# Optimization experiments

Measured on AMD Instinct MI355X. Metric: run time of the kernel, lower is better.

## Reference

```python
import jax, jax.numpy as jnp
import numpy as np

N_NODES = 100000
N_EDGES = 1600000
IN_C = 128
HID_C = 128
OUT_C = 64
N_GRAPHS = 64


def setup_inputs() -> dict:
    key = jax.random.key(0)
    ks = jax.random.split(key, 12)
    x = jax.random.normal(ks[0], (N_NODES, IN_C), dtype=jnp.float32)
    edge_index = jax.random.randint(ks[1], (2, N_EDGES), 0, N_NODES, dtype=jnp.int64)
    batch = jnp.sort(jax.random.randint(ks[2], (N_NODES,), 0, N_GRAPHS, dtype=jnp.int64))
    def glorot(k, fan_in, fan_out):
        s = jnp.sqrt(6.0 / (fan_in + fan_out))
        return jax.random.uniform(k, (fan_in, fan_out), jnp.float32, -s, s)
    W1 = glorot(ks[3], IN_C, HID_C);  b1 = jnp.zeros((HID_C,), jnp.float32)
    W2 = glorot(ks[4], HID_C, HID_C); b2 = jnp.zeros((HID_C,), jnp.float32)
    W3 = glorot(ks[5], HID_C, HID_C); b3 = jnp.zeros((HID_C,), jnp.float32)
    Wlin = glorot(ks[6], HID_C, OUT_C)
    blin = jnp.zeros((OUT_C,), jnp.float32)
    return {"x": x, "edge_index": edge_index, "batch": batch,
            "W1": W1, "b1": b1, "W2": W2, "b2": b2, "W3": W3, "b3": b3,
            "Wlin": Wlin, "blin": blin}


def _gcn_conv(x, W, b, src, dst, norm):
    # PyG GCNConv: h = x @ W; out[dst] += norm * h[src]; out += b
    h = x @ W
    msg = h[src] * norm[:, None]                     # [E+N, C] edge-wise gather (memory-bound)
    out = jax.ops.segment_sum(msg, dst, num_segments=N_NODES)
    return out + b


def reference(x, edge_index, batch, W1, b1, W2, b2, W3, b3, Wlin, blin):
    # add self-loops (PyG default add_self_loops=True)
    loops = jnp.arange(N_NODES, dtype=edge_index.dtype)
    src = jnp.concatenate([edge_index[0], loops])
    dst = jnp.concatenate([edge_index[1], loops])
    # symmetric normalization: deg over dst with unit edge weights
    deg = jax.ops.segment_sum(jnp.ones_like(src, dtype=x.dtype), dst, num_segments=N_NODES)
    dinv = jnp.where(deg > 0, jax.lax.rsqrt(deg), 0.0)
    norm = dinv[src] * dinv[dst]                     # [E+N]

    h = jax.nn.relu(_gcn_conv(x, W1, b1, src, dst, norm))
    h = jax.nn.relu(_gcn_conv(h, W2, b2, src, dst, norm))
    h = jax.nn.relu(_gcn_conv(h, W3, b3, src, dst, norm))

    # global mean pool over graphs
    sums = jax.ops.segment_sum(h, batch, num_segments=N_GRAPHS)
    cnts = jax.ops.segment_sum(jnp.ones((N_NODES,), h.dtype), batch, num_segments=N_GRAPHS)
    pooled = sums / jnp.clip(cnts, 1.0)[:, None]     # [G, HID_C]
    return pooled @ Wlin + blin                      # [G, OUT_C]
```

## Files before the change

### kernel.cpp

```cpp
#include <hip/hip_runtime.h>
#include <stdint.h>

#define C_HID 128
#define NGRAPH 64
#define COUT 64
#define POOL_S 64
#define NBLK 256
#define BKT 256
#define NBUK_MAX 512
#define SCAN_CH 4096

typedef short bf16x8 __attribute__((ext_vector_type(8)));
typedef float f32x4 __attribute__((ext_vector_type(4)));
typedef float f32x2 __attribute__((ext_vector_type(2)));

__device__ __forceinline__ unsigned short f2bf(float f){
  unsigned int u = __builtin_bit_cast(unsigned int, f);
  u = u + 0x7FFFu + ((u >> 16) & 1u);
  return (unsigned short)(u >> 16);
}
__device__ __forceinline__ float bflo(unsigned int u){
  return __builtin_bit_cast(float, u << 16);
}
__device__ __forceinline__ float bfhi(unsigned int u){
  return __builtin_bit_cast(float, u & 0xFFFF0000u);
}
__device__ __forceinline__ int clampi(int v, int lo, int hi){
  return v < lo ? lo : (v > hi ? hi : v);
}

__global__ void k_zero(float* __restrict__ out, int n){
  int i = blockIdx.x*blockDim.x + threadIdx.x;
  if (i < n) out[i] = 0.f;
}

__global__ __launch_bounds__(256) void k_cnt(const int* __restrict__ dst,
                                             int* __restrict__ cntg,
                                             int E, int N, int NBUK, int chunk){
  __shared__ int cnt[NBUK_MAX];
  int blk = blockIdx.x, t = threadIdx.x;
  for (int b = t; b < NBUK; b += 256) cnt[b] = 0;
  __syncthreads();
  int e0 = blk*chunk, e1 = min(E, e0 + chunk);
  for (int e = e0 + t; e < e1; e += 256)
    atomicAdd(&cnt[clampi(dst[e], 0, N-1) >> 8], 1);
  __syncthreads();
  for (int b = t; b < NBUK; b += 256)
    cntg[b*NBLK + blk] = cnt[b];
}

__global__ __launch_bounds__(256) void k_scanA(const int* __restrict__ cnt,
                                               int* __restrict__ bsum, int n){
  __shared__ int red[256];
  int blk = blockIdx.x, t = threadIdx.x;
  int base = blk*SCAN_CH + t*16;
  int s = 0;
  #pragma unroll
  for (int j = 0; j < 16; ++j){ int i = base + j; s += (i < n) ? cnt[i] : 0; }
  red[t] = s; __syncthreads();
  for (int off = 128; off > 0; off >>= 1){
    if (t < off) red[t] += red[t + off];
    __syncthreads();
  }
  if (t == 0) bsum[blk] = red[0];
}

__global__ __launch_bounds__(256) void k_scanB(const int* __restrict__ bsum,
                                               int* __restrict__ bbase,
                                               int* __restrict__ bases, int nb, int n){
  __shared__ int buf[256];
  int t = threadIdx.x;
  int v = (t < nb) ? bsum[t] : 0;
  buf[t] = v; __syncthreads();
  for (int off = 1; off < 256; off <<= 1){
    int add = (t >= off) ? buf[t-off] : 0;
    __syncthreads();
    buf[t] += add;
    __syncthreads();
  }
  if (t < nb) bbase[t] = buf[t] - v;
  if (t == nb-1) bases[n] = buf[t];
}

__global__ __launch_bounds__(256) void k_scanC(const int* __restrict__ cnt,
                                               const int* __restrict__ bbase,
                                               int* __restrict__ bases, int n){
  __shared__ int buf[256];
  int blk = blockIdx.x, t = threadIdx.x;
  int base = blk*SCAN_CH + t*16;
  int loc[16]; int s = 0;
  #pragma unroll
  for (int j = 0; j < 16; ++j){ int i = base + j; loc[j] = (i < n) ? cnt[i] : 0; s += loc[j]; }
  buf[t] = s; __syncthreads();
  for (int off = 1; off < 256; off <<= 1){
    int add = (t >= off) ? buf[t-off] : 0;
    __syncthreads();
    buf[t] += add;
    __syncthreads();
  }
  int run = bbase[blk] + buf[t] - s;
  #pragma unroll
  for (int j = 0; j < 16; ++j){
    int i = base + j;
    if (i < n) bases[i] = run;
    run += loc[j];
  }
}

__global__ __launch_bounds__(256) void k_scat(const int* __restrict__ src,
                                              const int* __restrict__ dst,
                                              const int* __restrict__ bases,
                                              unsigned int* __restrict__ rec,
                                              int E, int N, int NBUK, int chunk){
  __shared__ int cur[NBUK_MAX];
  int blk = blockIdx.x, t = threadIdx.x;
  for (int b = t; b < NBUK; b += 256) cur[b] = bases[b*NBLK + blk];
  __syncthreads();
  int e0 = blk*chunk, e1 = min(E, e0 + chunk);
  for (int e = e0 + t; e < e1; e += 256){
    int d = clampi(dst[e], 0, N-1);
    int s = clampi(src[e], 0, N-1);
    int p = atomicAdd(&cur[d >> 8], 1);
    rec[p] = (unsigned int)s | ((unsigned int)(d & 255) << 24);
  }
}

__global__ __launch_bounds__(256) void k_csr(const unsigned int* __restrict__ rec,
                                             const int* __restrict__ bases,
                                             int* __restrict__ offs, float* __restrict__ dinv,
                                             int* __restrict__ meta, int E, int N, int NBUK){
  __shared__ int cnt[BKT], loff[BKT], cur[BKT];
  int b = blockIdx.x, t = threadIdx.x;
  cnt[t] = 0;
  __syncthreads();
  int r0 = bases[b*NBLK];
  int r1 = (b+1 < NBUK) ? bases[(b+1)*NBLK] : E;
  for (int i = r0 + t; i < r1; i += 256)
    atomicAdd(&cnt[rec[i] >> 24], 1);
  __syncthreads();
  loff[t] = cnt[t];
  __syncthreads();
  for (int off = 1; off < BKT; off <<= 1){
    int add = (t >= off) ? loff[t - off] : 0;
    __syncthreads();
    loff[t] += add;
    __syncthreads();
  }
  int excl = loff[t] - cnt[t];
  cur[t] = r0 + excl;
  int node = b*BKT + t;
  if (node < N){
    offs[node] = r0 + excl;
    dinv[node] = rsqrtf((float)(cnt[t] + 1));
  }
  if (b == NBUK-1 && t == 0) offs[N] = E;
  __syncthreads();
  for (int i = r0 + t; i < r1; i += 256){
    unsigned int r = rec[i];
    int p = atomicAdd(&cur[r >> 24], 1);
    meta[p] = (int)(r & 0x00FFFFFFu);
  }
}

__global__ void k_xcast(const float2* __restrict__ x, const float* __restrict__ dinv,
                        unsigned short* __restrict__ y, unsigned short* __restrict__ y2, int N){
  int i = blockIdx.x*256 + threadIdx.x;
  int tot = N*64;
  if (i < tot){
    float2 v = x[i];
    float dn = dinv[i >> 6] * 64.f;
    int p = __builtin_amdgcn_cvt_pk_fp8_f32(v.x*dn, v.y*dn, 0, false);
    y[i] = (unsigned short)(p & 0xFFFF);
  } else if (i < tot + 64){
    y[i] = 0;
    y2[i] = 0;
  }
}

__global__ void k_prep(const float* __restrict__ W1, const float* __restrict__ W2,
                       const float* __restrict__ W3, unsigned short* __restrict__ Wt){
  int idx = blockIdx.x*256 + threadIdx.x;
  int w = idx >> 14;
  int r = idx & 16383;
  int n = r & 127, k = r >> 7;
  const float* W = (w == 0) ? W1 : (w == 1) ? W2 : W3;
  Wt[(size_t)w*16384 + (size_t)n*128 + k] = f2bf(W[k*128 + n]);
}

__global__ __launch_bounds__(256) void k_spmm(const unsigned short* __restrict__ y,
                       const int* __restrict__ offs,
                       const float* __restrict__ dinv,
                       const int* __restrict__ meta,
                       unsigned int* __restrict__ agg, int N){
  int wv   = __builtin_amdgcn_readfirstlane(threadIdx.x >> 6);
  int lane = threadIdx.x & 63;
  int g = lane >> 4, c = lane & 15;
  int node0 = blockIdx.x*16 + wv*4;
  if (node0 >= N) return;

  int eA = offs[node0];
  int eB = offs[min(node0+1, N)];
  int eC = offs[min(node0+2, N)];
  int eD = offs[min(node0+3, N)];
  int eE = offs[min(node0+4, N)];
  int c0 = eB-eA, c1 = eC-eB, c2 = eD-eC, c3 = eE-eD;
  int maxc = max(max(c0,c1), max(c2,c3));

  int e0l  = (g==0) ? eA : (g==1) ? eB : (g==2) ? eC : eD;
  int cntl = (g==0) ? c0 : (g==1) ? c1 : (g==2) ? c2 : c3;
  int nodeg = node0 + g;
  bool nok = nodeg < N;
  int nself = nok ? nodeg : N;

  const uint2* yrow = (const uint2*)y;

  int mv0 = (c < cntl)      ? meta[e0l + c]      : N;
  int mv1 = (c + 16 < cntl) ? meta[e0l + c + 16] : N;
  uint2 us = yrow[(size_t)nself*16 + c];
  float dl = dinv[nok ? nodeg : 0];

  f32x2 acc[4];
  { f32x2 f;
    f = __builtin_amdgcn_cvt_pk_f32_fp8((int)us.x, false); acc[0] = f;
    f = __builtin_amdgcn_cvt_pk_f32_fp8((int)us.x, true);  acc[1] = f;
    f = __builtin_amdgcn_cvt_pk_f32_fp8((int)us.y, false); acc[2] = f;
    f = __builtin_amdgcn_cvt_pk_f32_fp8((int)us.y, true);  acc[3] = f; }

  uint2 u[8];
#define SWZ0(J) __builtin_amdgcn_ds_swizzle(mv0, (0x10 | (((J)&15)<<5)))
#define SWZ1(J) __builtin_amdgcn_ds_swizzle(mv1, (0x10 | (((J)&15)<<5)))
#define GA(K, SM) u[K] = yrow[(size_t)(unsigned)(SM)*16 + c]
#define CONV8() do{ _Pragma("unroll") \
  for (int k2 = 0; k2 < 8; ++k2){ \
    f32x2 f; \
    f = __builtin_amdgcn_cvt_pk_f32_fp8((int)u[k2].x, false); acc[0] += f; \
    f = __builtin_amdgcn_cvt_pk_f32_fp8((int)u[k2].x, true);  acc[1] += f; \
    f = __builtin_amdgcn_cvt_pk_f32_fp8((int)u[k2].y, false); acc[2] += f; \
    f = __builtin_amdgcn_cvt_pk_f32_fp8((int)u[k2].y, true);  acc[3] += f; } }while(0)

  if (0 < maxc){
    GA(0,SWZ0(0)); GA(1,SWZ0(1)); GA(2,SWZ0(2)); GA(3,SWZ0(3));
    GA(4,SWZ0(4)); GA(5,SWZ0(5)); GA(6,SWZ0(6)); GA(7,SWZ0(7));
    __builtin_amdgcn_sched_barrier(0);
    CONV8();
  }
  if (8 < maxc){
    GA(0,SWZ0(8)); GA(1,SWZ0(9)); GA(2,SWZ0(10)); GA(3,SWZ0(11));
    GA(4,SWZ0(12)); GA(5,SWZ0(13)); GA(6,SWZ0(14)); GA(7,SWZ0(15));
    __builtin_amdgcn_sched_barrier(0);
    CONV8();
  }
  if (16 < maxc){
    GA(0,SWZ1(16)); GA(1,SWZ1(17)); GA(2,SWZ1(18)); GA(3,SWZ1(19));
    GA(4,SWZ1(20)); GA(5,SWZ1(21)); GA(6,SWZ1(22)); GA(7,SWZ1(23));
    __builtin_amdgcn_sched_barrier(0);
    CONV8();
  }
  if (24 < maxc){
    GA(0,SWZ1(24)); GA(1,SWZ1(25)); GA(2,SWZ1(26)); GA(3,SWZ1(27));
    GA(4,SWZ1(28)); GA(5,SWZ1(29)); GA(6,SWZ1(30)); GA(7,SWZ1(31));
    __builtin_amdgcn_sched_barrier(0);
    CONV8();
  }
#undef SWZ0
#undef SWZ1
#undef GA
#undef CONV8

  for (int j = 32; j < maxc; ++j){
    int sm = (j < cntl) ? meta[e0l + j] : N;
    uint2 t = yrow[(size_t)(unsigned)sm*16 + c];
    f32x2 f;
    f = __builtin_amdgcn_cvt_pk_f32_fp8((int)t.x, false); acc[0] += f;
    f = __builtin_amdgcn_cvt_pk_f32_fp8((int)t.x, true);  acc[1] += f;
    f = __builtin_amdgcn_cvt_pk_f32_fp8((int)t.y, false); acc[2] += f;
    f = __builtin_amdgcn_cvt_pk_f32_fp8((int)t.y, true);  acc[3] += f;
  }

  float dn = dl * 0.015625f;
  if (nok){
    uint4 w;
    w.x = (unsigned int)f2bf(acc[0].x*dn) | ((unsigned int)f2bf(acc[0].y*dn) << 16);
    w.y = (unsigned int)f2bf(acc[1].x*dn) | ((unsigned int)f2bf(acc[1].y*dn) << 16);
    w.z = (unsigned int)f2bf(acc[2].x*dn) | ((unsigned int)f2bf(acc[2].y*dn) << 16);
    w.w = (unsigned int)f2bf(acc[3].x*dn) | ((unsigned int)f2bf(acc[3].y*dn) << 16);
    *(uint4*)(agg + (size_t)nodeg*64 + c*4) = w;
  }
}

#define GEMM_BLOCKS 512
template<bool FP8OUT>
__global__ __launch_bounds__(256) void k_gemm(const unsigned short* __restrict__ A,
                                              const unsigned short* __restrict__ Wt,
                                              const float* __restrict__ bias,
                                              const float* __restrict__ scale,
                                              void* __restrict__ outv, int M){
  __shared__ unsigned short wt[128*136];
  {
    const uint4* wsrc = (const uint4*)Wt;
    for (int i = threadIdx.x; i < 4096; i += 256){
      uint4 v = wsrc[i];
      int n = i >> 4, kblk = i & 15;
      *(uint4*)&wt[n*136 + kblk*8] = v;
    }
  }
  __syncthreads();

  int wv = threadIdx.x >> 6, lane = threadIdx.x & 63;
  int q = lane >> 4, ln = lane & 15;
  int tiles = (M + 63) >> 6;

  for (int tile = blockIdx.x; tile < tiles; tile += GEMM_BLOCKS){
    int m0 = tile*64 + wv*16;
    int arow = m0 + ln;
    bool arow_ok = (arow < M);
    int arow_s = arow_ok ? arow : 0;

    f32x4 zero = {0.f, 0.f, 0.f, 0.f};
    f32x4 acc[8];
    #pragma unroll
    for (int t = 0; t < 8; ++t) acc[t] = zero;

    #pragma unroll
    for (int kk = 0; kk < 4; ++kk){
      bf16x8 a;
      if (arow_ok){
        __builtin_memcpy(&a, A + (size_t)arow_s*128 + kk*32 + q*8, 16);
      } else {
        a = (bf16x8){0,0,0,0,0,0,0,0};
      }
      #pragma unroll
      for (int t = 0; t < 8; ++t){
        bf16x8 b;
        __builtin_memcpy(&b, &wt[(t*16 + ln)*136 + kk*32 + q*8], 16);
        acc[t] = __builtin_amdgcn_mfma_f32_16x16x32_bf16(a, b, acc[t], 0, 0, 0);
      }
    }
    float sc[4];
    #pragma unroll
    for (int r = 0; r < 4; ++r){
      int row = m0 + q*4 + r;
      sc[r] = (FP8OUT && row < M) ? scale[row] * 64.f : 1.0f;
    }
    #pragma unroll
    for (int t = 0; t < 8; ++t){
      float bv = bias[t*16 + ln];
      #pragma unroll
      for (int r = 0; r < 4; ++r){
        int row = m0 + q*4 + r;
        if (row < M){
          float v = acc[t][r] + bv;
          v = v > 0.f ? v : 0.f;
          if (FP8OUT){
            v *= sc[r];
            int p = __builtin_amdgcn_cvt_pk_fp8_f32(v, v, 0, false);
            ((unsigned char*)outv)[(size_t)row*128 + t*16 + ln] = (unsigned char)(p & 0xFF);
          } else {
            ((unsigned short*)outv)[(size_t)row*128 + t*16 + ln] = f2bf(v);
          }
        }
      }
    }
  }
}

__device__ __forceinline__ int lower_bound_i(const int* arr, int n, int val){
  int lo = 0, hi = n;
  while (lo < hi){ int mid = (lo + hi) >> 1; if (arr[mid] < val) lo = mid + 1; else hi = mid; }
  return lo;
}

__global__ void k_pool(const unsigned int* __restrict__ x, const int* __restrict__ batch,
                       float* __restrict__ partial, int N){
  int g = blockIdx.x / POOL_S, s = blockIdx.x % POOL_S;
  int h = threadIdx.x >> 6;
  int lane = threadIdx.x & 63;
  int rs = clampi(lower_bound_i(batch, N, g), 0, N);
  int re = clampi(lower_bound_i(batch, N, g + 1), rs, N);
  int len = re - rs;
  int a = rs + (int)(((long long)len * s) / POOL_S);
  int b = rs + (int)(((long long)len * (s + 1)) / POOL_S);
  float ax = 0.f, ay = 0.f;
  for (int i = a + h; i < b; i += 2){
    unsigned int u = x[(size_t)i*64 + lane];
    ax += bflo(u);
    ay += bfhi(u);
  }
  float* p = partial + ((size_t)(g*POOL_S + s)*2 + h)*C_HID;
  p[2*lane]   = ax;
  p[2*lane+1] = ay;
}

__global__ void k_final(const float* __restrict__ partial, const int* __restrict__ batch,
                        const float* __restrict__ Wl, const float* __restrict__ bl,
                        float* __restrict__ out, int N){
  __shared__ float sums[C_HID];
  int g = blockIdx.x;
  int t = threadIdx.x;
  float acc = 0.f;
  const float* p = partial + (size_t)g*POOL_S*2*C_HID;
  for (int j = 0; j < POOL_S*2; ++j)
    acc += p[j*C_HID + t];
  sums[t] = acc;
  __syncthreads();
  if (t < COUT){
    int rs = clampi(lower_bound_i(batch, N, g), 0, N);
    int re = clampi(lower_bound_i(batch, N, g + 1), rs, N);
    float inv = 1.0f / fmaxf((float)(re - rs), 1.0f);
    float o = 0.f;
    for (int k = 0; k < 128; ++k)
      o += sums[k] * Wl[k*COUT + t];
    out[g*COUT + t] = o * inv + bl[t];
  }
}

extern "C" void kernel_launch(void* const* d_in, const int* in_sizes, int n_in,
                              void* d_out, int out_size, void* d_ws, size_t ws_size,
                              hipStream_t stream){
  const float* x0 = (const float*)d_in[0];
  const int* ei   = (const int*)d_in[1];
  const int* batch= (const int*)d_in[2];
  const float* W1 = (const float*)d_in[3];
  const float* b1 = (const float*)d_in[4];
  const float* W2 = (const float*)d_in[5];
  const float* b2 = (const float*)d_in[6];
  const float* W3 = (const float*)d_in[7];
  const float* b3 = (const float*)d_in[8];
  const float* Wl = (const float*)d_in[9];
  const float* bl = (const float*)d_in[10];
  float* out = (float*)d_out;

  int E = in_sizes[1] / 2;
  int N = in_sizes[2];
  const int* src = ei;
  const int* dst = ei + E;
  int NBUK = (N + BKT - 1) / BKT;
  int chunk = (E + NBLK - 1) / NBLK;
  int ncnt = NBUK * NBLK;
  int nsb  = (ncnt + SCAN_CH - 1) / SCAN_CH;

  size_t off_acc = 0;
  auto carve = [&](size_t bytes)->size_t{
    size_t r = off_acc; off_acc += (bytes + 255) & ~(size_t)255; return r;
  };
  size_t o_cnt   = carve((size_t)ncnt*4);
  size_t o_bases = carve((size_t)(ncnt+1)*4);
  size_t o_bsum  = carve(256*4);
  size_t o_bbase = carve(256*4);
  size_t o_offs  = carve((size_t)(N+1)*4);
  size_t o_dinv  = carve((size_t)N*4);
  size_t o_meta  = carve((size_t)E*4);
  size_t o_rec   = carve((size_t)E*4);
  size_t o_yA    = carve((size_t)(N+1)*C_HID);
  size_t o_yB    = carve((size_t)(N+1)*C_HID);
  size_t o_aggb  = carve((size_t)N*C_HID*2);
  size_t o_wt    = carve((size_t)3*128*128*2);
  size_t need = off_acc;

  size_t hbuf_avail = o_aggb - o_meta;
  bool alias_ok = hbuf_avail >= (size_t)N*C_HID*2;
  alias_ok = alias_ok &&
             ((size_t)(N+1)*C_HID >= (size_t)NGRAPH*POOL_S*2*C_HID*4);

  if (ws_size < need || NBUK > NBUK_MAX || nsb > 256 || !alias_ok){
    k_zero<<<(out_size+255)/256, 256, 0, stream>>>(out, out_size);
    return;
  }

  char* base = (char*)d_ws;
  int* cntg  = (int*)(base + o_cnt);
  int* bases = (int*)(base + o_bases);
  int* bsum  = (int*)(base + o_bsum);
  int* bbase = (int*)(base + o_bbase);
  int* offs  = (int*)(base + o_offs);
  float* dinv= (float*)(base + o_dinv);
  int* meta  = (int*)(base + o_meta);
  unsigned int* rec   = (unsigned int*)(base + o_rec);
  unsigned short* yA  = (unsigned short*)(base + o_yA);
  unsigned short* yB  = (unsigned short*)(base + o_yB);
  unsigned int* aggb  = (unsigned int*)(base + o_aggb);
  unsigned short* wt  = (unsigned short*)(base + o_wt);
  unsigned short* hbuf= (unsigned short*)(base + o_meta);
  float* part         = (float*)(base + o_yB);

  k_cnt  <<<NBLK, 256, 0, stream>>>(dst, cntg, E, N, NBUK, chunk);
  k_scanA<<<nsb, 256, 0, stream>>>(cntg, bsum, ncnt);
  k_scanB<<<1, 256, 0, stream>>>(bsum, bbase, bases, nsb, ncnt);
  k_scanC<<<nsb, 256, 0, stream>>>(cntg, bbase, bases, ncnt);
  k_scat <<<NBLK, 256, 0, stream>>>(src, dst, bases, rec, E, N, NBUK, chunk);
  k_csr  <<<NBUK, BKT, 0, stream>>>(rec, bases, offs, dinv, meta, E, N, NBUK);

  k_xcast<<<(N*64 + 64 + 255)/256, 256, 0, stream>>>((const float2*)x0, dinv, yA, yB, N);
  k_prep <<<192, 256, 0, stream>>>(W1, W2, W3, wt);

  int spmm_grid = (N + 15) / 16;

  k_spmm<<<spmm_grid, 256, 0, stream>>>(yA, offs, dinv, meta, aggb, N);
  k_gemm<true ><<<GEMM_BLOCKS, 256, 0, stream>>>((const unsigned short*)aggb, wt,           b1, dinv, (void*)yB, N);
  k_spmm<<<spmm_grid, 256, 0, stream>>>(yB, offs, dinv, meta, aggb, N);
  k_gemm<true ><<<GEMM_BLOCKS, 256, 0, stream>>>((const unsigned short*)aggb, wt + 16384,   b2, dinv, (void*)yA, N);
  k_spmm<<<spmm_grid, 256, 0, stream>>>(yA, offs, dinv, meta, aggb, N);
  k_gemm<false><<<GEMM_BLOCKS, 256, 0, stream>>>((const unsigned short*)aggb, wt + 2*16384, b3, dinv, (void*)hbuf, N);

  k_pool <<<NGRAPH*POOL_S, 128, 0, stream>>>((const unsigned int*)hbuf, batch, part, N);
  k_final<<<NGRAPH, 128, 0, stream>>>(part, batch, Wl, bl, out, N);
}
```

Baseline: 338.0 us.

## Fuse SpMM aggregation with dense GEMM per 64-node tile via shared memory

Merges the per-layer sparse aggregation kernel and the bf16 MFMA GEMM kernel into one kernel. Each block aggregates 64 nodes into a shared-memory A tile, then multiplies it by the weight matrix read directly from global memory (no LDS staging of W). This removes the bf16 aggregate round-trip through global memory and half the launches, at the cost of per-block uncoalesced weight reads and a block-wide sync between gather and MFMA phases. hbuf now gets its own workspace slot instead of aliasing meta.

```diff
diff --git a/kernel.cpp b/kernel.cpp
--- a/kernel.cpp
+++ b/kernel.cpp
@@ -187,46 +187,50 @@
   Wt[(size_t)w*16384 + (size_t)n*128 + k] = f2bf(W[k*128 + n]);
 }
 
-__global__ __launch_bounds__(256) void k_spmm(const unsigned short* __restrict__ y,
+template<bool FP8OUT>
+__global__ __launch_bounds__(256) void k_fused(const unsigned short* __restrict__ y,
                        const int* __restrict__ offs,
                        const float* __restrict__ dinv,
                        const int* __restrict__ meta,
-                       unsigned int* __restrict__ agg, int N){
+                       const unsigned short* __restrict__ Wt,
+                       const float* __restrict__ bias,
+                       void* __restrict__ outv, int N){
+  __shared__ unsigned short As[64*136];
   int wv   = __builtin_amdgcn_readfirstlane(threadIdx.x >> 6);
   int lane = threadIdx.x & 63;
   int g = lane >> 4, c = lane & 15;
-  int node0 = blockIdx.x*16 + wv*4;
-  if (node0 >= N) return;
-
-  int eA = offs[node0];
-  int eB = offs[min(node0+1, N)];
-  int eC = offs[min(node0+2, N)];
-  int eD = offs[min(node0+3, N)];
-  int eE = offs[min(node0+4, N)];
-  int c0 = eB-eA, c1 = eC-eB, c2 = eD-eC, c3 = eE-eD;
-  int maxc = max(max(c0,c1), max(c2,c3));
-
-  int e0l  = (g==0) ? eA : (g==1) ? eB : (g==2) ? eC : eD;
-  int cntl = (g==0) ? c0 : (g==1) ? c1 : (g==2) ? c2 : c3;
-  int nodeg = node0 + g;
-  bool nok = nodeg < N;
-  int nself = nok ? nodeg : N;
-
+  int tile0 = blockIdx.x*64;
   const uint2* yrow = (const uint2*)y;
 
-  int mv0 = (c < cntl)      ? meta[e0l + c]      : N;
-  int mv1 = (c + 16 < cntl) ? meta[e0l + c + 16] : N;
-  uint2 us = yrow[(size_t)nself*16 + c];
-  float dl = dinv[nok ? nodeg : 0];
-
-  f32x2 acc[4];
-  { f32x2 f;
-    f = __builtin_amdgcn_cvt_pk_f32_fp8((int)us.x, false); acc[0] = f;
-    f = __builtin_amdgcn_cvt_pk_f32_fp8((int)us.x, true);  acc[1] = f;
-    f = __builtin_amdgcn_cvt_pk_f32_fp8((int)us.y, false); acc[2] = f;
-    f = __builtin_amdgcn_cvt_pk_f32_fp8((int)us.y, true);  acc[3] = f; }
-
-  uint2 u[8];
+  for (int b4 = 0; b4 < 4; ++b4){
+    int node0 = tile0 + wv*16 + b4*4;
+    int eA = offs[min(node0,   N)];
+    int eB = offs[min(node0+1, N)];
+    int eC = offs[min(node0+2, N)];
+    int eD = offs[min(node0+3, N)];
+    int eE = offs[min(node0+4, N)];
+    int c0 = eB-eA, c1 = eC-eB, c2 = eD-eC, c3 = eE-eD;
+    int maxc = max(max(c0,c1), max(c2,c3));
+
+    int e0l  = (g==0) ? eA : (g==1) ? eB : (g==2) ? eC : eD;
+    int cntl = (g==0) ? c0 : (g==1) ? c1 : (g==2) ? c2 : c3;
+    int nodeg = node0 + g;
+    bool nok = nodeg < N;
+    int nself = nok ? nodeg : N;
+
+    int mv0 = (c < cntl)      ? meta[e0l + c]      : N;
+    int mv1 = (c + 16 < cntl) ? meta[e0l + c + 16] : N;
+    uint2 us = yrow[(size_t)nself*16 + c];
+    float dl = dinv[nok ? nodeg : 0];
+
+    f32x2 acc[4];
+    { f32x2 f;
+      f = __builtin_amdgcn_cvt_pk_f32_fp8((int)us.x, false); acc[0] = f;
+      f = __builtin_amdgcn_cvt_pk_f32_fp8((int)us.x, true);  acc[1] = f;
+      f = __builtin_amdgcn_cvt_pk_f32_fp8((int)us.y, false); acc[2] = f;
+      f = __builtin_amdgcn_cvt_pk_f32_fp8((int)us.y, true);  acc[3] = f; }
+
+    uint2 u[8];
 #define SWZ0(J) __builtin_amdgcn_ds_swizzle(mv0, (0x10 | (((J)&15)<<5)))
 #define SWZ1(J) __builtin_amdgcn_ds_swizzle(mv1, (0x10 | (((J)&15)<<5)))
 #define GA(K, SM) u[K] = yrow[(size_t)(unsigned)(SM)*16 + c]
@@ -238,126 +242,96 @@
     f = __builtin_amdgcn_cvt_pk_f32_fp8((int)u[k2].y, false); acc[2] += f; \
     f = __builtin_amdgcn_cvt_pk_f32_fp8((int)u[k2].y, true);  acc[3] += f; } }while(0)
 
-  if (0 < maxc){
-    GA(0,SWZ0(0)); GA(1,SWZ0(1)); GA(2,SWZ0(2)); GA(3,SWZ0(3));
-    GA(4,SWZ0(4)); GA(5,SWZ0(5)); GA(6,SWZ0(6)); GA(7,SWZ0(7));
-    __builtin_amdgcn_sched_barrier(0);
-    CONV8();
-  }
-  if (8 < maxc){
-    GA(0,SWZ0(8)); GA(1,SWZ0(9)); GA(2,SWZ0(10)); GA(3,SWZ0(11));
-    GA(4,SWZ0(12)); GA(5,SWZ0(13)); GA(6,SWZ0(14)); GA(7,SWZ0(15));
-    __builtin_amdgcn_sched_barrier(0);
-    CONV8();
-  }
-  if (16 < maxc){
-    GA(0,SWZ1(16)); GA(1,SWZ1(17)); GA(2,SWZ1(18)); GA(3,SWZ1(19));
-    GA(4,SWZ1(20)); GA(5,SWZ1(21)); GA(6,SWZ1(22)); GA(7,SWZ1(23));
-    __builtin_amdgcn_sched_barrier(0);
-    CONV8();
-  }
-  if (24 < maxc){
-    GA(0,SWZ1(24)); GA(1,SWZ1(25)); GA(2,SWZ1(26)); GA(3,SWZ1(27));
-    GA(4,SWZ1(28)); GA(5,SWZ1(29)); GA(6,SWZ1(30)); GA(7,SWZ1(31));
-    __builtin_amdgcn_sched_barrier(0);
-    CONV8();
-  }
+    if (0 < maxc){
+      GA(0,SWZ0(0)); GA(1,SWZ0(1)); GA(2,SWZ0(2)); GA(3,SWZ0(3));
+      GA(4,SWZ0(4)); GA(5,SWZ0(5)); GA(6,SWZ0(6)); GA(7,SWZ0(7));
+      __builtin_amdgcn_sched_barrier(0);
+      CONV8();
+    }
+    if (8 < maxc){
+      GA(0,SWZ0(8)); GA(1,SWZ0(9)); GA(2,SWZ0(10)); GA(3,SWZ0(11));
+      GA(4,SWZ0(12)); GA(5,SWZ0(13)); GA(6,SWZ0(14)); GA(7,SWZ0(15));
+      __builtin_amdgcn_sched_barrier(0);
+      CONV8();
+    }
+    if (16 < maxc){
+      GA(0,SWZ1(16)); GA(1,SWZ1(17)); GA(2,SWZ1(18)); GA(3,SWZ1(19));
+      GA(4,SWZ1(20)); GA(5,SWZ1(21)); GA(6,SWZ1(22)); GA(7,SWZ1(23));
+      __builtin_amdgcn_sched_barrier(0);
+      CONV8();
+    }
+    if (24 < maxc){
+      GA(0,SWZ1(24)); GA(1,SWZ1(25)); GA(2,SWZ1(26)); GA(3,SWZ1(27));
+      GA(4,SWZ1(28)); GA(5,SWZ1(29)); GA(6,SWZ1(30)); GA(7,SWZ1(31));
+      __builtin_amdgcn_sched_barrier(0);
+      CONV8();
+    }
 #undef SWZ0
 #undef SWZ1
 #undef GA
 #undef CONV8
 
-  for (int j = 32; j < maxc; ++j){
-    int sm = (j < cntl) ? meta[e0l + j] : N;
-    uint2 t = yrow[(size_t)(unsigned)sm*16 + c];
-    f32x2 f;
-    f = __builtin_amdgcn_cvt_pk_f32_fp8((int)t.x, false); acc[0] += f;
-    f = __builtin_amdgcn_cvt_pk_f32_fp8((int)t.x, true);  acc[1] += f;
-    f = __builtin_amdgcn_cvt_pk_f32_fp8((int)t.y, false); acc[2] += f;
-    f = __builtin_amdgcn_cvt_pk_f32_fp8((int)t.y, true);  acc[3] += f;
-  }
-
-  float dn = dl * 0.015625f;
-  if (nok){
-    uint4 w;
-    w.x = (unsigned int)f2bf(acc[0].x*dn) | ((unsigned int)f2bf(acc[0].y*dn) << 16);
-    w.y = (unsigned int)f2bf(acc[1].x*dn) | ((unsigned int)f2bf(acc[1].y*dn) << 16);
-    w.z = (unsigned int)f2bf(acc[2].x*dn) | ((unsigned int)f2bf(acc[2].y*dn) << 16);
-    w.w = (unsigned int)f2bf(acc[3].x*dn) | ((unsigned int)f2bf(acc[3].y*dn) << 16);
-    *(uint4*)(agg + (size_t)nodeg*64 + c*4) = w;
-  }
-}
-
-#define GEMM_BLOCKS 512
-template<bool FP8OUT>
-__global__ __launch_bounds__(256) void k_gemm(const unsigned short* __restrict__ A,
-                                              const unsigned short* __restrict__ Wt,
-                                              const float* __restrict__ bias,
-                                              const float* __restrict__ scale,
-                                              void* __restrict__ outv, int M){
-  __shared__ unsigned short wt[128*136];
-  {
-    const uint4* wsrc = (const uint4*)Wt;
-    for (int i = threadIdx.x; i < 4096; i += 256){
-      uint4 v = wsrc[i];
-      int n = i >> 4, kblk = i & 15;
-      *(uint4*)&wt[n*136 + kblk*8] = v;
-    }
-  }
-  __syncthreads();
-
-  int wv = threadIdx.x >> 6, lane = threadIdx.x & 63;
-  int q = lane >> 4, ln = lane & 15;
-  int tiles = (M + 63) >> 6;
-
-  for (int tile = blockIdx.x; tile < tiles; tile += GEMM_BLOCKS){
-    int m0 = tile*64 + wv*16;
-    int arow = m0 + ln;
-    bool arow_ok = (arow < M);
-    int arow_s = arow_ok ? arow : 0;
-
-    f32x4 zero = {0.f, 0.f, 0.f, 0.f};
-    f32x4 acc[8];
+    for (int j = 32; j < maxc; ++j){
+      int sm = (j < cntl) ? meta[e0l + j] : N;
+      uint2 t = yrow[(size_t)(unsigned)sm*16 + c];
+      f32x2 f;
+      f = __builtin_amdgcn_cvt_pk_f32_fp8((int)t.x, false); acc[0] += f;
+      f = __builtin_amdgcn_cvt_pk_f32_fp8((int)t.x, true);  acc[1] += f;
+      f = __builtin_amdgcn_cvt_pk_f32_fp8((int)t.y, false); acc[2] += f;
+      f = __builtin_amdgcn_cvt_pk_f32_fp8((int)t.y, true);  acc[3] += f;
+    }
+
+    float dn = dl * 0.015625f;
+    uint4 w = {0u, 0u, 0u, 0u};
+    if (nok){
+      w.x = (unsigned int)f2bf(acc[0].x*dn) | ((unsigned int)f2bf(acc[0].y*dn) << 16);
+      w.y = (unsigned int)f2bf(acc[1].x*dn) | ((unsigned int)f2bf(acc[1].y*dn) << 16);
+      w.z = (unsigned int)f2bf(acc[2].x*dn) | ((unsigned int)f2bf(acc[2].y*dn) << 16);
+      w.w = (unsigned int)f2bf(acc[3].x*dn) | ((unsigned int)f2bf(acc[3].y*dn) << 16);
+    }
+    *(uint4*)&As[(size_t)(wv*16 + b4*4 + g)*136 + c*8] = w;
+  }
+  __syncthreads();
+
+  int q = g, ln = c;
+  f32x4 zero = {0.f, 0.f, 0.f, 0.f};
+  f32x4 acc[8];
+  #pragma unroll
+  for (int t = 0; t < 8; ++t) acc[t] = zero;
+
+  #pragma unroll
+  for (int kk = 0; kk < 4; ++kk){
+    bf16x8 a;
+    __builtin_memcpy(&a, &As[(size_t)(wv*16 + ln)*136 + kk*32 + q*8], 16);
     #pragma unroll
-    for (int t = 0; t < 8; ++t) acc[t] = zero;
-
-    #pragma unroll
-    for (int kk = 0; kk < 4; ++kk){
-      bf16x8 a;
-      if (arow_ok){
-        __builtin_memcpy(&a, A + (size_t)arow_s*128 + kk*32 + q*8, 16);
-      } else {
-        a = (bf16x8){0,0,0,0,0,0,0,0};
-      }
-      #pragma unroll
-      for (int t = 0; t < 8; ++t){
-        bf16x8 b;
-        __builtin_memcpy(&b, &wt[(t*16 + ln)*136 + kk*32 + q*8], 16);
-        acc[t] = __builtin_amdgcn_mfma_f32_16x16x32_bf16(a, b, acc[t], 0, 0, 0);
-      }
-    }
-    float sc[4];
+    for (int t = 0; t < 8; ++t){
+      bf16x8 b;
+      __builtin_memcpy(&b, Wt + (size_t)(t*16 + ln)*128 + kk*32 + q*8, 16);
+      acc[t] = __builtin_amdgcn_mfma_f32_16x16x32_bf16(a, b, acc[t], 0, 0, 0);
+    }
+  }
+  int m0 = tile0 + wv*16;
+  float sc[4];
+  #pragma unroll
+  for (int r = 0; r < 4; ++r){
+    int row = m0 + q*4 + r;
+    sc[r] = (FP8OUT && row < N) ? dinv[row] * 64.f : 1.0f;
+  }
+  #pragma unroll
+  for (int t = 0; t < 8; ++t){
+    float bv = bias[t*16 + ln];
     #pragma unroll
     for (int r = 0; r < 4; ++r){
       int row = m0 + q*4 + r;
-      sc[r] = (FP8OUT && row < M) ? scale[row] * 64.f : 1.0f;
-    }
-    #pragma unroll
-    for (int t = 0; t < 8; ++t){
-      float bv = bias[t*16 + ln];
-      #pragma unroll
-      for (int r = 0; r < 4; ++r){
-        int row = m0 + q*4 + r;
-        if (row < M){
-          float v = acc[t][r] + bv;
-          v = v > 0.f ? v : 0.f;
-          if (FP8OUT){
-            v *= sc[r];
-            int p = __builtin_amdgcn_cvt_pk_fp8_f32(v, v, 0, false);
-            ((unsigned char*)outv)[(size_t)row*128 + t*16 + ln] = (unsigned char)(p & 0xFF);
-          } else {
-            ((unsigned short*)outv)[(size_t)row*128 + t*16 + ln] = f2bf(v);
-          }
+      if (row < N){
+        float v = acc[t][r] + bv;
+        v = v > 0.f ? v : 0.f;
+        if (FP8OUT){
+          v *= sc[r];
+          int p = __builtin_amdgcn_cvt_pk_fp8_f32(v, v, 0, false);
+          ((unsigned char*)outv)[(size_t)row*128 + t*16 + ln] = (unsigned char)(p & 0xFF);
+        } else {
+          ((unsigned short*)outv)[(size_t)row*128 + t*16 + ln] = f2bf(v);
         }
       }
     }
@@ -453,14 +427,12 @@
   size_t o_rec   = carve((size_t)E*4);
   size_t o_yA    = carve((size_t)(N+1)*C_HID);
   size_t o_yB    = carve((size_t)(N+1)*C_HID);
-  size_t o_aggb  = carve((size_t)N*C_HID*2);
+  size_t o_hbuf  = carve((size_t)N*C_HID*2);
   size_t o_wt    = carve((size_t)3*128*128*2);
   size_t need = off_acc;
 
-  size_t hbuf_avail = o_aggb - o_meta;
-  bool alias_ok = hbuf_avail >= (size_t)N*C_HID*2;
-  alias_ok = alias_ok &&
-             ((size_t)(N+1)*C_HID >= (size_t)NGRAPH*POOL_S*2*C_HID*4);
+  bool alias_ok =
+      ((size_t)(N+1)*C_HID >= (size_t)NGRAPH*POOL_S*2*C_HID*4);
 
   if (ws_size < need || NBUK > NBUK_MAX || nsb > 256 || !alias_ok){
     k_zero<<<(out_size+255)/256, 256, 0, stream>>>(out, out_size);
@@ -478,9 +450,8 @@
   unsigned int* rec   = (unsigned int*)(base + o_rec);
   unsigned short* yA  = (unsigned short*)(base + o_yA);
   unsigned short* yB  = (unsigned short*)(base + o_yB);
-  unsigned int* aggb  = (unsigned int*)(base + o_aggb);
+  unsigned short* hbuf= (unsigned short*)(base + o_hbuf);
   unsigned short* wt  = (unsigned short*)(base + o_wt);
-  unsigned short* hbuf= (unsigned short*)(base + o_meta);
   float* part         = (float*)(base + o_yB);
 
   k_cnt  <<<NBLK, 256, 0, stream>>>(dst, cntg, E, N, NBUK, chunk);
@@ -493,14 +464,11 @@
   k_xcast<<<(N*64 + 64 + 255)/256, 256, 0, stream>>>((const float2*)x0, dinv, yA, yB, N);
   k_prep <<<192, 256, 0, stream>>>(W1, W2, W3, wt);
 
-  int spmm_grid = (N + 15) / 16;
-
-  k_spmm<<<spmm_grid, 256, 0, stream>>>(yA, offs, dinv, meta, aggb, N);
-  k_gemm<true ><<<GEMM_BLOCKS, 256, 0, stream>>>((const unsigned short*)aggb, wt,           b1, dinv, (void*)yB, N);
-  k_spmm<<<spmm_grid, 256, 0, stream>>>(yB, offs, dinv, meta, aggb, N);
-  k_gemm<true ><<<GEMM_BLOCKS, 256, 0, stream>>>((const unsigned short*)aggb, wt + 16384,   b2, dinv, (void*)yA, N);
-  k_spmm<<<spmm_grid, 256, 0, stream>>>(yA, offs, dinv, meta, aggb, N);
-  k_gemm<false><<<GEMM_BLOCKS, 256, 0, stream>>>((const unsigned short*)aggb, wt + 2*16384, b3, dinv, (void*)hbuf, N);
+  int fgrid = (N + 63) / 64;
+
+  k_fused<true ><<<fgrid, 256, 0, stream>>>(yA, offs, dinv, meta, wt,           b1, (void*)yB,   N);
+  k_fused<true ><<<fgrid, 256, 0, stream>>>(yB, offs, dinv, meta, wt + 16384,   b2, (void*)yA,   N);
+  k_fused<false><<<fgrid, 256, 0, stream>>>(yA, offs, dinv, meta, wt + 2*16384, b3, (void*)hbuf, N);
 
   k_pool <<<NGRAPH*POOL_S, 128, 0, stream>>>((const unsigned int*)hbuf, batch, part, N);
   k_final<<<NGRAPH, 128, 0, stream>>>(part, batch, Wl, bl, out, N);
```

Measured after the change: 383.5 us. +13.5%, slower.
